# Kernel tuning notes

Measured on AMD Instinct MI355X. Metric: run time of the kernel, lower is better.

Reference implementation:

```python
import jax, jax.numpy as jnp
import numpy as np

# Sampled-neighborhood sizes (NeighborSampler-style shrinking hops)
N0, N1, N2, N3 = 200000, 50000, 12500, 3200
E0, E1, E2 = 500000, 125000, 32000
D_IN, D_H, D_OUT = 128, 256, 128


def setup_inputs() -> dict:
    key = jax.random.key(0)
    ks = jax.random.split(key, 16)
    x = jax.random.normal(ks[0], (N0, D_IN), dtype=jnp.float32)
    src0 = jax.random.randint(ks[1], (E0,), 0, N0)
    dst0 = jax.random.randint(ks[2], (E0,), 0, N1)
    src1 = jax.random.randint(ks[3], (E1,), 0, N1)
    dst1 = jax.random.randint(ks[4], (E1,), 0, N2)
    src2 = jax.random.randint(ks[5], (E2,), 0, N2)
    dst2 = jax.random.randint(ks[6], (E2,), 0, N3)
    s = 0.05
    # SAGEConv params: lin_l (applied to aggregated neighbors, has bias), lin_r (root)
    wl0 = jax.random.normal(ks[7], (D_H, D_IN), dtype=jnp.float32) * s
    wr0 = jax.random.normal(ks[8], (D_H, D_IN), dtype=jnp.float32) * s
    b0 = jnp.zeros((D_H,), dtype=jnp.float32)
    wl1 = jax.random.normal(ks[9], (D_H, D_H), dtype=jnp.float32) * s
    wr1 = jax.random.normal(ks[10], (D_H, D_H), dtype=jnp.float32) * s
    b1 = jnp.zeros((D_H,), dtype=jnp.float32)
    wl2 = jax.random.normal(ks[11], (D_OUT, D_H), dtype=jnp.float32) * s
    wr2 = jax.random.normal(ks[12], (D_OUT, D_H), dtype=jnp.float32) * s
    b2 = jnp.zeros((D_OUT,), dtype=jnp.float32)
    return {"x": x, "src0": src0, "dst0": dst0, "src1": src1, "dst1": dst1,
            "src2": src2, "dst2": dst2,
            "wl0": wl0, "wr0": wr0, "b0": b0,
            "wl1": wl1, "wr1": wr1, "b1": b1,
            "wl2": wl2, "wr2": wr2, "b2": b2}


def _sage(x, src, dst, n_tgt, wl, wr, b):
    """Bipartite SAGEConv with mean aggregation (PyG default)."""
    x_tgt = x[:n_tgt]                                   # [n_tgt, d_in]
    msg = x[src]                                        # [E, d_in] gather
    s = jax.ops.segment_sum(msg, dst, num_segments=n_tgt)
    cnt = jax.ops.segment_sum(jnp.ones((src.shape[0], 1), x.dtype), dst,
                              num_segments=n_tgt)
    mean = s / jnp.maximum(cnt, 1.0)                    # mean over in-neighbors
    return mean @ wl.T + b + x_tgt @ wr.T               # [n_tgt, d_out]


def reference(x, src0, dst0, src1, dst1, src2, dst2,
              wl0, wr0, b0, wl1, wr1, b1, wl2, wr2, b2):
    h = jax.nn.relu(_sage(x, src0, dst0, N1, wl0, wr0, b0))
    h = jax.nn.relu(_sage(h, src1, dst1, N2, wl1, wr1, b1))
    return _sage(h, src2, dst2, N3, wl2, wr2, b2)       # [N3, D_OUT]
```

## Files before the change

kernel.cpp:

```cpp
#include <hip/hip_runtime.h>

#define N0s 200000
#define N1s 50000
#define N2s 12500
#define N3s 3200
#define E0s 500000
#define E1s 125000
#define E2s 32000
#define D_INs 128
#define D_Hs 256
#define D_OUTs 128

#define CAP 64
#define LOGCAP 6

#define GSTRIDE 72

#define XN4 (N0s * D_INs / 4)
#define WN4 65536
#define CAST_TOTAL (XN4 + WN4)
#define CAST_BLOCKS ((CAST_TOTAL + 2047) / 2048)
#define FILL_BLOCKS ((E0s + E1s + E2s + 255) / 256)

typedef __attribute__((ext_vector_type(8))) short short8;
typedef __attribute__((ext_vector_type(8))) unsigned short ushort8;
typedef __attribute__((ext_vector_type(4))) float floatx4;

__device__ __forceinline__ unsigned short f32_to_bf16_rne(float f) {
    unsigned int u = __float_as_uint(f);
    u += 0x7fffu + ((u >> 16) & 1u);
    return (unsigned short)(u >> 16);
}
__device__ __forceinline__ float bf16_to_f32(unsigned short h) {
    return __uint_as_float(((unsigned int)h) << 16);
}

struct PrepArgs {
    const float* x; unsigned short* xb;
    const float* ws_[6]; unsigned short* wd[6];
    const int *src0, *dst0, *src1, *dst1, *src2, *dst2;
    int *cnt0, *cnt1, *cnt2;
    int *eidx0, *eidx1, *eidx2;
};

__launch_bounds__(256)
__global__ void prep(PrepArgs a)
{
    if (blockIdx.x < FILL_BLOCKS) {
        int e = blockIdx.x * 256 + threadIdx.x;
        if (e < E0s) {
            int d = a.dst0[e];
            int p = atomicAdd(&a.cnt0[d], 1);
            if (p < CAP) a.eidx0[(d << LOGCAP) + p] = a.src0[e];
        } else if (e < E0s + E1s) {
            int i = e - E0s;
            int d = a.dst1[i];
            int p = atomicAdd(&a.cnt1[d], 1);
            if (p < CAP) a.eidx1[(d << LOGCAP) + p] = a.src1[i];
        } else if (e < E0s + E1s + E2s) {
            int i = e - E0s - E1s;
            int d = a.dst2[i];
            int p = atomicAdd(&a.cnt2[d], 1);
            if (p < CAP) a.eidx2[(d << LOGCAP) + p] = a.src2[i];
        }
        return;
    }
    int cb = blockIdx.x - FILL_BLOCKS;
    #pragma unroll
    for (int j = 0; j < 8; ++j) {
        int i = cb * 2048 + j * 256 + threadIdx.x;
        if (i < XN4) {
            float4 v = *(const float4*)&a.x[(size_t)i * 4];
            ushort4 o;
            o.x = f32_to_bf16_rne(v.x);
            o.y = f32_to_bf16_rne(v.y);
            o.z = f32_to_bf16_rne(v.z);
            o.w = f32_to_bf16_rne(v.w);
            *(ushort4*)&a.xb[(size_t)i * 4] = o;
        } else if (i < CAST_TOTAL) {
            int g = i - XN4;
            int seg, base;
            if      (g < 8192)  { seg = 0; base = 0; }
            else if (g < 16384) { seg = 1; base = 8192; }
            else if (g < 32768) { seg = 2; base = 16384; }
            else if (g < 49152) { seg = 3; base = 32768; }
            else if (g < 57344) { seg = 4; base = 49152; }
            else                { seg = 5; base = 57344; }
            int k = g - base;
            float4 v = *(const float4*)&a.ws_[seg][(size_t)k * 4];
            ushort4 o;
            o.x = f32_to_bf16_rne(v.x);
            o.y = f32_to_bf16_rne(v.y);
            o.z = f32_to_bf16_rne(v.z);
            o.w = f32_to_bf16_rne(v.w);
            *(ushort4*)&a.wd[seg][(size_t)k * 4] = o;
        }
    }
}

__launch_bounds__(256)
__global__ void gather_mean(const unsigned short* __restrict__ X,
                            const int* __restrict__ eidx,
                            const int* __restrict__ cnt,
                            unsigned short* __restrict__ out,
                            int n_tgt, int D, int shift)
{
    int gid = blockIdx.x * 256 + threadIdx.x;
    int row = gid >> shift;
    if (row >= n_tgt) return;
    int c = (gid & ((1 << shift) - 1)) << 3;

    int deg = cnt[row];
    int e = min(deg, CAP);
    const int* bp = &eidx[row << LOGCAP];

    float acc[8];
    #pragma unroll
    for (int j = 0; j < 8; ++j) acc[j] = 0.f;

    int i = 0;
    for (; i + 4 <= e; i += 4) {
        int4 ss = *(const int4*)&bp[i];
        ushort8 v0 = *(const ushort8*)&X[(size_t)ss.x * D + c];
        ushort8 v1 = *(const ushort8*)&X[(size_t)ss.y * D + c];
        ushort8 v2 = *(const ushort8*)&X[(size_t)ss.z * D + c];
        ushort8 v3 = *(const ushort8*)&X[(size_t)ss.w * D + c];
        #pragma unroll
        for (int j = 0; j < 8; ++j)
            acc[j] += (bf16_to_f32(v0[j]) + bf16_to_f32(v1[j]))
                    + (bf16_to_f32(v2[j]) + bf16_to_f32(v3[j]));
    }
    for (; i < e; ++i) {
        ushort8 v0 = *(const ushort8*)&X[(size_t)bp[i] * D + c];
        #pragma unroll
        for (int j = 0; j < 8; ++j) acc[j] += bf16_to_f32(v0[j]);
    }

    float inv = 1.0f / fmaxf((float)deg, 1.0f);
    ushort8 o;
    #pragma unroll
    for (int j = 0; j < 8; ++j) o[j] = f32_to_bf16_rne(acc[j] * inv);
    *(ushort8*)&out[(size_t)row * D + c] = o;
}

template<int BM, int BN, int OUT_BF16, int RELU>
__launch_bounds__(256)
__global__ void mfma_gemm_t(const unsigned short* __restrict__ A1,
                            const unsigned short* __restrict__ A2,
                            const unsigned short* __restrict__ W1,
                            const unsigned short* __restrict__ W2,
                            const float* __restrict__ bias,
                            void* __restrict__ Cout,
                            int M, int N, int K1, int K2)
{
    constexpr int MT = BM / 32;
    constexpr int NT = BN / 32;
    constexpr int AITER = BM / 32;
    constexpr int CS = BN + 4;

    __shared__ unsigned short smem[2 * BM * GSTRIDE];
    unsigned short* As = smem;
    unsigned short* Bs = smem + BM * GSTRIDE;

    const int tid  = threadIdx.x;
    const int wave = tid >> 6;
    const int lane = tid & 63;
    const int quad = lane >> 4;
    const int lr   = lane & 15;
    const int wm   = wave >> 1;
    const int wn   = wave & 1;
    const int row0 = blockIdx.x * BM;
    const int col0 = blockIdx.y * BN;

    floatx4 acc[MT][NT] = {};

    for (int seg = 0; seg < 2; ++seg) {
        const unsigned short* Ap = (seg == 0) ? A1 : A2;
        const unsigned short* Wp = (seg == 0) ? W1 : W2;
        const int K = (seg == 0) ? K1 : K2;

        for (int k0 = 0; k0 < K; k0 += 64) {
            #pragma unroll
            for (int it = 0; it < AITER; ++it) {
                int sid = tid + it * 256;
                int r = sid >> 3;
                int sc = (sid & 7) << 3;
                int gr = min(row0 + r, M - 1);
                uint4 v = *(const uint4*)&Ap[(size_t)gr * K + k0 + sc];
                *(uint4*)&As[r * GSTRIDE + sc] = v;
            }
            #pragma unroll
            for (int it = 0; it < AITER; ++it) {
                int sid = tid + it * 256;
                int r = sid >> 3;
                int sc = (sid & 7) << 3;
                uint4 v = *(const uint4*)&Wp[(size_t)(col0 + r) * K + k0 + sc];
                *(uint4*)&Bs[r * GSTRIDE + sc] = v;
            }
            __syncthreads();

            #pragma unroll
            for (int kh = 0; kh < 2; ++kh) {
                short8 afr[MT], bfr[NT];
                #pragma unroll
                for (int mt = 0; mt < MT; ++mt)
                    afr[mt] = *(const short8*)&As[(wm * (BM/2) + mt * 16 + lr) * GSTRIDE + kh * 32 + quad * 8];
                #pragma unroll
                for (int nt = 0; nt < NT; ++nt)
                    bfr[nt] = *(const short8*)&Bs[(wn * (BN/2) + nt * 16 + lr) * GSTRIDE + kh * 32 + quad * 8];

                #pragma unroll
                for (int mt = 0; mt < MT; ++mt)
                    #pragma unroll
                    for (int nt = 0; nt < NT; ++nt)
                        acc[mt][nt] = __builtin_amdgcn_mfma_f32_16x16x32_bf16(
                            afr[mt], bfr[nt], acc[mt][nt], 0, 0, 0);
            }
            __syncthreads();
        }
    }

    if (OUT_BF16) {
        unsigned short* Cs = smem;
        #pragma unroll
        for (int nt = 0; nt < NT; ++nt) {
            int col = wn * (BN/2) + nt * 16 + lr;
            float bv = bias[col0 + col];
            #pragma unroll
            for (int mt = 0; mt < MT; ++mt) {
                #pragma unroll
                for (int reg = 0; reg < 4; ++reg) {
                    int row = wm * (BM/2) + mt * 16 + quad * 4 + reg;
                    float v = acc[mt][nt][reg] + bv;
                    if (RELU) v = fmaxf(v, 0.f);
                    Cs[row * CS + col] = f32_to_bf16_rne(v);
                }
            }
        }
        __syncthreads();
        constexpr int TPRO = 256 / BM;
        constexpr int SPT  = BN / TPRO;
        int r  = tid / TPRO;
        int hf = tid % TPRO;
        int gr = row0 + r;
        if (gr < M) {
            unsigned short* Crow = (unsigned short*)Cout + (size_t)gr * N + col0 + hf * SPT;
            #pragma unroll
            for (int j = 0; j < SPT / 8; ++j) {
                uint4 v = *(const uint4*)&Cs[r * CS + hf * SPT + j * 8];
                *(uint4*)&Crow[j * 8] = v;
            }
        }
    } else {
        #pragma unroll
        for (int nt = 0; nt < NT; ++nt) {
            int gc = col0 + wn * (BN/2) + nt * 16 + lr;
            float bv = bias[gc];
            #pragma unroll
            for (int mt = 0; mt < MT; ++mt) {
                #pragma unroll
                for (int reg = 0; reg < 4; ++reg) {
                    int gr = row0 + wm * (BM/2) + mt * 16 + quad * 4 + reg;
                    if (gr < M) {
                        float v = acc[mt][nt][reg] + bv;
                        if (RELU) v = fmaxf(v, 0.f);
                        ((float*)Cout)[(size_t)gr * N + gc] = v;
                    }
                }
            }
        }
    }
}

extern "C" void kernel_launch(void* const* d_in, const int* in_sizes, int n_in,
                              void* d_out, int out_size, void* d_ws, size_t ws_size,
                              hipStream_t stream)
{
    const float* x   = (const float*)d_in[0];
    const int* src0  = (const int*)d_in[1];
    const int* dst0  = (const int*)d_in[2];
    const int* src1  = (const int*)d_in[3];
    const int* dst1  = (const int*)d_in[4];
    const int* src2  = (const int*)d_in[5];
    const int* dst2  = (const int*)d_in[6];
    const float* wl0 = (const float*)d_in[7];
    const float* wr0 = (const float*)d_in[8];
    const float* b0  = (const float*)d_in[9];
    const float* wl1 = (const float*)d_in[10];
    const float* wr1 = (const float*)d_in[11];
    const float* b1  = (const float*)d_in[12];
    const float* wl2 = (const float*)d_in[13];
    const float* wr2 = (const float*)d_in[14];
    const float* b2  = (const float*)d_in[15];

    unsigned short* ws = (unsigned short*)d_ws;
    unsigned short* xb    = ws;
    unsigned short* h1    = xb + (size_t)N0s * D_INs;
    unsigned short* h2    = h1 + (size_t)N1s * D_Hs;
    unsigned short* meanA = h2 + (size_t)N2s * D_Hs;
    unsigned short* wl0b  = meanA + (size_t)N1s * D_INs;
    unsigned short* wr0b  = wl0b + 32768;
    unsigned short* wl1b  = wr0b + 32768;
    unsigned short* wr1b  = wl1b + 65536;
    unsigned short* wl2b  = wr1b + 65536;
    unsigned short* wr2b  = wl2b + 32768;
    int* ib = (int*)(wr2b + 32768);
    int* cnt0 = ib;
    int* cnt1 = cnt0 + 50048;
    int* cnt2 = cnt1 + 12544;
    int* eidx0 = cnt2 + 3264;
    int* eidx1 = eidx0 + (size_t)N1s * CAP;
    int* eidx2 = eidx1 + (size_t)N2s * CAP;

    PrepArgs pa;
    pa.x = x; pa.xb = xb;
    pa.ws_[0] = wl0; pa.ws_[1] = wr0; pa.ws_[2] = wl1;
    pa.ws_[3] = wr1; pa.ws_[4] = wl2; pa.ws_[5] = wr2;
    pa.wd[0] = wl0b; pa.wd[1] = wr0b; pa.wd[2] = wl1b;
    pa.wd[3] = wr1b; pa.wd[4] = wl2b; pa.wd[5] = wr2b;
    pa.src0 = src0; pa.dst0 = dst0; pa.src1 = src1; pa.dst1 = dst1;
    pa.src2 = src2; pa.dst2 = dst2;
    pa.cnt0 = cnt0; pa.cnt1 = cnt1; pa.cnt2 = cnt2;
    pa.eidx0 = eidx0; pa.eidx1 = eidx1; pa.eidx2 = eidx2;

    hipMemsetAsync(cnt0, 0, (50048 + 12544 + 3264) * sizeof(int), stream);
    prep<<<FILL_BLOCKS + CAST_BLOCKS, 256, 0, stream>>>(pa);

    {
        int th = N1s * 16;
        gather_mean<<<(th + 255) / 256, 256, 0, stream>>>(xb, eidx0, cnt0,
                                                          meanA, N1s, D_INs, 4);
        dim3 g((N1s + 127) / 128, D_Hs / 128);
        mfma_gemm_t<128,128,1,1><<<g, 256, 0, stream>>>(meanA, xb, wl0b, wr0b, b0, h1,
                                                        N1s, D_Hs, D_INs, D_INs);
    }
    {
        int th = N2s * 32;
        gather_mean<<<(th + 255) / 256, 256, 0, stream>>>(h1, eidx1, cnt1,
                                                          meanA, N2s, D_Hs, 5);
        dim3 g((N2s + 63) / 64, D_Hs / 64);
        mfma_gemm_t<64,64,1,1><<<g, 256, 0, stream>>>(meanA, h1, wl1b, wr1b, b1, h2,
                                                      N2s, D_Hs, D_Hs, D_Hs);
    }
    {
        int th = N3s * 32;
        gather_mean<<<(th + 255) / 256, 256, 0, stream>>>(h2, eidx2, cnt2,
                                                          meanA, N3s, D_Hs, 5);
        dim3 g((N3s + 63) / 64, D_OUTs / 64);
        mfma_gemm_t<64,64,0,0><<<g, 256, 0, stream>>>(meanA, h2, wl2b, wr2b, b2, (float*)d_out,
                                                      N3s, D_OUTs, D_Hs, D_Hs);
    }
}
```

Baseline: 318.3 us.

## Cast only root rows of x and gather layer-0 neighbors directly from fp32

Stops converting all 200k rows of x to bf16 and converts only the first N1 rows that the root GEMM needs. The layer-0 gather now reads fp32 x directly and accumulates means in fp32. The single prep kernel is split into separate fill and cast kernels. This removes a full read and write pass over x, at the cost of fp32 gather traffic twice as large per row and one extra kernel launch.

```diff
diff --git a/kernel.cpp b/kernel.cpp
--- a/kernel.cpp
+++ b/kernel.cpp
@@ -16,11 +16,10 @@
 
 #define GSTRIDE 72
 
-#define XN4 (N0s * D_INs / 4)
+#define XS4 (N1s * D_INs / 4)
 #define WN4 65536
-#define CAST_TOTAL (XN4 + WN4)
-#define CAST_BLOCKS ((CAST_TOTAL + 2047) / 2048)
-#define FILL_BLOCKS ((E0s + E1s + E2s + 255) / 256)
+#define CSMALL_TOTAL (XS4 + WN4)
+#define CSMALL_BLOCKS ((CSMALL_TOTAL + 2047) / 2048)
 
 typedef __attribute__((ext_vector_type(8))) short short8;
 typedef __attribute__((ext_vector_type(8))) unsigned short ushort8;
@@ -35,41 +34,45 @@
     return __uint_as_float(((unsigned int)h) << 16);
 }
 
-struct PrepArgs {
-    const float* x; unsigned short* xb;
-    const float* ws_[6]; unsigned short* wd[6];
+struct Bins {
     const int *src0, *dst0, *src1, *dst1, *src2, *dst2;
     int *cnt0, *cnt1, *cnt2;
     int *eidx0, *eidx1, *eidx2;
 };
 
 __launch_bounds__(256)
-__global__ void prep(PrepArgs a)
-{
-    if (blockIdx.x < FILL_BLOCKS) {
-        int e = blockIdx.x * 256 + threadIdx.x;
-        if (e < E0s) {
-            int d = a.dst0[e];
-            int p = atomicAdd(&a.cnt0[d], 1);
-            if (p < CAP) a.eidx0[(d << LOGCAP) + p] = a.src0[e];
-        } else if (e < E0s + E1s) {
-            int i = e - E0s;
-            int d = a.dst1[i];
-            int p = atomicAdd(&a.cnt1[d], 1);
-            if (p < CAP) a.eidx1[(d << LOGCAP) + p] = a.src1[i];
-        } else if (e < E0s + E1s + E2s) {
-            int i = e - E0s - E1s;
-            int d = a.dst2[i];
-            int p = atomicAdd(&a.cnt2[d], 1);
-            if (p < CAP) a.eidx2[(d << LOGCAP) + p] = a.src2[i];
-        }
-        return;
-    }
-    int cb = blockIdx.x - FILL_BLOCKS;
+__global__ void fill3(Bins b)
+{
+    int e = blockIdx.x * 256 + threadIdx.x;
+    if (e < E0s) {
+        int d = b.dst0[e];
+        int p = atomicAdd(&b.cnt0[d], 1);
+        if (p < CAP) b.eidx0[(d << LOGCAP) + p] = b.src0[e];
+    } else if (e < E0s + E1s) {
+        int i = e - E0s;
+        int d = b.dst1[i];
+        int p = atomicAdd(&b.cnt1[d], 1);
+        if (p < CAP) b.eidx1[(d << LOGCAP) + p] = b.src1[i];
+    } else if (e < E0s + E1s + E2s) {
+        int i = e - E0s - E1s;
+        int d = b.dst2[i];
+        int p = atomicAdd(&b.cnt2[d], 1);
+        if (p < CAP) b.eidx2[(d << LOGCAP) + p] = b.src2[i];
+    }
+}
+
+struct CastArgs {
+    const float* x; unsigned short* xb;
+    const float* ws_[6]; unsigned short* wd[6];
+};
+
+__launch_bounds__(256)
+__global__ void cast_small(CastArgs a)
+{
     #pragma unroll
     for (int j = 0; j < 8; ++j) {
-        int i = cb * 2048 + j * 256 + threadIdx.x;
-        if (i < XN4) {
+        int i = blockIdx.x * 2048 + j * 256 + threadIdx.x;
+        if (i < XS4) {
             float4 v = *(const float4*)&a.x[(size_t)i * 4];
             ushort4 o;
             o.x = f32_to_bf16_rne(v.x);
@@ -77,8 +80,8 @@
             o.z = f32_to_bf16_rne(v.z);
             o.w = f32_to_bf16_rne(v.w);
             *(ushort4*)&a.xb[(size_t)i * 4] = o;
-        } else if (i < CAST_TOTAL) {
-            int g = i - XN4;
+        } else if (i < CSMALL_TOTAL) {
+            int g = i - XS4;
             int seg, base;
             if      (g < 8192)  { seg = 0; base = 0; }
             else if (g < 16384) { seg = 1; base = 8192; }
@@ -96,6 +99,48 @@
             *(ushort4*)&a.wd[seg][(size_t)k * 4] = o;
         }
     }
+}
+
+__launch_bounds__(256)
+__global__ void gather_mean_f32(const float* __restrict__ X,
+                                const int* __restrict__ eidx,
+                                const int* __restrict__ cnt,
+                                unsigned short* __restrict__ out,
+                                int n_tgt)
+{
+    int gid = blockIdx.x * 256 + threadIdx.x;
+    int row = gid >> 5;
+    if (row >= n_tgt) return;
+    int c = (gid & 31) << 2;
+
+    int deg = cnt[row];
+    int e = min(deg, CAP);
+    const int* bp = &eidx[row << LOGCAP];
+
+    float a0 = 0.f, a1 = 0.f, a2 = 0.f, a3 = 0.f;
+    int i = 0;
+    for (; i + 4 <= e; i += 4) {
+        int4 ss = *(const int4*)&bp[i];
+        float4 v0 = *(const float4*)&X[(size_t)ss.x * D_INs + c];
+        float4 v1 = *(const float4*)&X[(size_t)ss.y * D_INs + c];
+        float4 v2 = *(const float4*)&X[(size_t)ss.z * D_INs + c];
+        float4 v3 = *(const float4*)&X[(size_t)ss.w * D_INs + c];
+        a0 += (v0.x + v1.x) + (v2.x + v3.x);
+        a1 += (v0.y + v1.y) + (v2.y + v3.y);
+        a2 += (v0.z + v1.z) + (v2.z + v3.z);
+        a3 += (v0.w + v1.w) + (v2.w + v3.w);
+    }
+    for (; i < e; ++i) {
+        float4 v = *(const float4*)&X[(size_t)bp[i] * D_INs + c];
+        a0 += v.x; a1 += v.y; a2 += v.z; a3 += v.w;
+    }
+    float inv = 1.0f / fmaxf((float)deg, 1.0f);
+    ushort4 o;
+    o.x = f32_to_bf16_rne(a0 * inv);
+    o.y = f32_to_bf16_rne(a1 * inv);
+    o.z = f32_to_bf16_rne(a2 * inv);
+    o.w = f32_to_bf16_rne(a3 * inv);
+    *(ushort4*)&out[(size_t)row * D_INs + c] = o;
 }
 
 __launch_bounds__(256)
@@ -312,24 +357,28 @@
     int* eidx1 = eidx0 + (size_t)N1s * CAP;
     int* eidx2 = eidx1 + (size_t)N2s * CAP;
 
-    PrepArgs pa;
-    pa.x = x; pa.xb = xb;
-    pa.ws_[0] = wl0; pa.ws_[1] = wr0; pa.ws_[2] = wl1;
-    pa.ws_[3] = wr1; pa.ws_[4] = wl2; pa.ws_[5] = wr2;
-    pa.wd[0] = wl0b; pa.wd[1] = wr0b; pa.wd[2] = wl1b;
-    pa.wd[3] = wr1b; pa.wd[4] = wl2b; pa.wd[5] = wr2b;
-    pa.src0 = src0; pa.dst0 = dst0; pa.src1 = src1; pa.dst1 = dst1;
-    pa.src2 = src2; pa.dst2 = dst2;
-    pa.cnt0 = cnt0; pa.cnt1 = cnt1; pa.cnt2 = cnt2;
-    pa.eidx0 = eidx0; pa.eidx1 = eidx1; pa.eidx2 = eidx2;
+    Bins b;
+    b.src0 = src0; b.dst0 = dst0; b.src1 = src1; b.dst1 = dst1;
+    b.src2 = src2; b.dst2 = dst2;
+    b.cnt0 = cnt0; b.cnt1 = cnt1; b.cnt2 = cnt2;
+    b.eidx0 = eidx0; b.eidx1 = eidx1; b.eidx2 = eidx2;
+
+    CastArgs ca;
+    ca.x = x; ca.xb = xb;
+    ca.ws_[0] = wl0; ca.ws_[1] = wr0; ca.ws_[2] = wl1;
+    ca.ws_[3] = wr1; ca.ws_[4] = wl2; ca.ws_[5] = wr2;
+    ca.wd[0] = wl0b; ca.wd[1] = wr0b; ca.wd[2] = wl1b;
+    ca.wd[3] = wr1b; ca.wd[4] = wl2b; ca.wd[5] = wr2b;
 
     hipMemsetAsync(cnt0, 0, (50048 + 12544 + 3264) * sizeof(int), stream);
-    prep<<<FILL_BLOCKS + CAST_BLOCKS, 256, 0, stream>>>(pa);
+    const int Etot = E0s + E1s + E2s;
+    fill3<<<(Etot + 255) / 256, 256, 0, stream>>>(b);
+    cast_small<<<CSMALL_BLOCKS, 256, 0, stream>>>(ca);
 
     {
-        int th = N1s * 16;
-        gather_mean<<<(th + 255) / 256, 256, 0, stream>>>(xb, eidx0, cnt0,
-                                                          meanA, N1s, D_INs, 4);
+        int th = N1s * 32;
+        gather_mean_f32<<<(th + 255) / 256, 256, 0, stream>>>(x, eidx0, cnt0,
+                                                              meanA, N1s);
         dim3 g((N1s + 127) / 128, D_Hs / 128);
         mfma_gemm_t<128,128,1,1><<<g, 256, 0, stream>>>(meanA, xb, wl0b, wr0b, b0, h1,
                                                         N1s, D_Hs, D_INs, D_INs);
```

Result: no change. 317.9 us (-0.1%).
